# Kernel tuning notes

Hardware: AMD Instinct MI355X
Metric: run time of the kernel (lower is better)

## Reference

```python
import jax, jax.numpy as jnp
import numpy as np

NUM_ITEMS = 50000
EMB = 16
SLATE = 10
HID = 512
LAT = 64
RESP = 1024
BATCH = 256


def _linear_params(k, out_dim, in_dim):
    kw, kb = jax.random.split(k)
    s = 1.0 / np.sqrt(in_dim)
    W = jax.random.uniform(kw, (out_dim, in_dim), jnp.float32, -s, s)
    b = jax.random.uniform(kb, (out_dim,), jnp.float32, -s, s)
    return W, b


def setup_inputs() -> dict:
    key = jax.random.key(0)
    ks = jax.random.split(key, 10)
    user_repr = jax.random.randint(ks[0], (BATCH, NUM_ITEMS), 0, 2, dtype=jnp.int32)
    slate = jax.random.randint(ks[1], (BATCH, SLATE), 0, NUM_ITEMS, dtype=jnp.int32)
    response_encoded = jax.random.uniform(ks[2], (BATCH, RESP), jnp.float32)
    eps = jax.random.normal(ks[3], (BATCH, LAT), jnp.float32)
    emb = jax.random.normal(ks[4], (NUM_ITEMS, EMB), jnp.float32)
    in_enc = SLATE * EMB + EMB + RESP
    W_enc, b_enc = _linear_params(ks[5], HID, in_enc)
    W_mu, b_mu = _linear_params(ks[6], LAT, HID)
    W_lv, b_lv = _linear_params(ks[7], LAT, HID)
    in_dec = LAT + EMB + RESP
    W_d1, b_d1 = _linear_params(ks[8], HID, in_dec)
    W_d2, b_d2 = _linear_params(ks[9], SLATE * EMB, HID)
    return {"user_repr": user_repr, "slate": slate, "response_encoded": response_encoded,
            "eps": eps, "emb": emb, "W_enc": W_enc, "b_enc": b_enc,
            "W_mu": W_mu, "b_mu": b_mu, "W_lv": W_lv, "b_lv": b_lv,
            "W_d1": W_d1, "b_d1": b_d1, "W_d2": W_d2, "b_d2": b_d2}


def reference(user_repr, slate, response_encoded, eps, emb,
              W_enc, b_enc, W_mu, b_mu, W_lv, b_lv, W_d1, b_d1, W_d2, b_d2):
    # Ragged embedding-mean pooling over interacted items (vectorized segment mean):
    # mean of emb rows where user_repr==1  ==  (indicator @ emb) / count
    uf = user_repr.astype(jnp.float32)                       # [B, N]
    counts = jnp.sum(uf, axis=1, keepdims=True)              # [B, 1]
    user = (uf @ emb) / counts                               # [B, E]

    cond = jnp.concatenate([user, response_encoded], axis=1)  # [B, E+R]
    slate_emb = emb[slate]                                    # [B, K, E]
    slate_vec = slate_emb.reshape(-1, SLATE * EMB)            # [B, K*E]
    x = jnp.concatenate([slate_vec, cond], axis=1)

    # encoder
    h = jax.nn.relu(x @ W_enc.T + b_enc)
    z_mean = h @ W_mu.T + b_mu
    z_log_var = h @ W_lv.T + b_lv

    # reparameterized sample
    z = z_mean + eps * jnp.exp(0.5 * z_log_var)

    # decoder
    dz = jnp.concatenate([z, cond], axis=1)
    dh = jax.nn.relu(dz @ W_d1.T + b_d1)
    rx = jax.nn.relu(dh @ W_d2.T + b_d2)                      # [B, K*E]
    rx = rx.reshape(-1, SLATE, EMB)                           # [B, K, E]

    # scores vs all items, softmax over items
    logits = jnp.einsum('bkh,nh->bkn', rx, emb)               # [B, K, N]
    probs = jax.nn.softmax(logits, axis=2)
    recon_slate = jnp.argmax(probs, axis=2)                   # [B, K]
    recon_resp = jnp.take_along_axis(probs, slate[:, :, None], axis=2)[..., 0]  # [B, K]
    return z_mean, z_log_var, recon_slate, recon_resp
```

## Files before the change

### kernel.cpp

```cpp
#include <hip/hip_runtime.h>

#define NITEMS 50000
#define EMBD   16
#define NSLATE 10
#define HIDD   512
#define LATD   64
#define RESPD  1024
#define BATCH  256
#define NPCH   25
#define PI4    500
#define BG     4
#define LOG2E  1.44269504088896340736f
#define SHIFT  64.0f

#define NCOL   2560
#define NT     1563
#define IC     224
#define TPC    7

#define OUT_ZM 0
#define OUT_ZLV 16384
#define OUT_RS 32768
#define OUT_RR 35328

#define WS_X    0
#define WS_DZ   307200
#define WS_P2   0
#define WS_PS   0
#define WS_KEY  573440
#define WS_PP   589824
#define WS_PART 589824
#define WS_RX   1114112
#define WS_RXS0 1155072
#define WS_RXS1 1175552
#define WS_RXS2 1196032

typedef __attribute__((ext_vector_type(8))) short bfrag;
typedef __attribute__((ext_vector_type(16))) float f32x16;

__device__ __forceinline__ float bfround(float v) {
  unsigned u = __float_as_uint(v);
  unsigned r = (u + 0x7FFFu + ((u >> 16) & 1u)) & 0xFFFF0000u;
  return __uint_as_float(r);
}

__device__ __forceinline__ unsigned mono32(float f) {
  unsigned u = __float_as_uint(f);
  return (u & 0x80000000u) ? ~u : (u | 0x80000000u);
}

#define FMAX3(a, b, c) fmaxf(fmaxf((a), (b)), (c))

__global__ __launch_bounds__(256) void pool_part(const int* __restrict__ u,
    const float* __restrict__ emb, float* __restrict__ pp) {
  int bg = blockIdx.x, c = blockIdx.y, t = threadIdx.x;
  float acc[BG][17];
  #pragma unroll
  for (int j = 0; j < BG; ++j)
    #pragma unroll
    for (int i = 0; i < 17; ++i) acc[j][i] = 0.0f;
  const int4* ub = (const int4*)u;
  size_t base = (size_t)(bg * BG) * 12500 + (size_t)c * PI4;
  int nBase = c * 2000;
  for (int i4 = t; i4 < PI4; i4 += 256) {
    int4 u0 = ub[base + i4];
    int4 u1 = ub[base + 12500 + i4];
    int4 u2 = ub[base + 25000 + i4];
    int4 u3 = ub[base + 37500 + i4];
    int w[BG][4] = {{u0.x, u0.y, u0.z, u0.w}, {u1.x, u1.y, u1.z, u1.w},
                    {u2.x, u2.y, u2.z, u2.w}, {u3.x, u3.y, u3.z, u3.w}};
    const float4* e4 = (const float4*)(emb + (size_t)(nBase + i4 * 4) * 16);
    #pragma unroll
    for (int it = 0; it < 4; ++it) {
      float4 ea = e4[it * 4 + 0], eb = e4[it * 4 + 1];
      float4 ec = e4[it * 4 + 2], ed = e4[it * 4 + 3];
      #pragma unroll
      for (int j = 0; j < BG; ++j) {
        float wf = (float)w[j][it];
        acc[j][0]  = fmaf(wf, ea.x, acc[j][0]);
        acc[j][1]  = fmaf(wf, ea.y, acc[j][1]);
        acc[j][2]  = fmaf(wf, ea.z, acc[j][2]);
        acc[j][3]  = fmaf(wf, ea.w, acc[j][3]);
        acc[j][4]  = fmaf(wf, eb.x, acc[j][4]);
        acc[j][5]  = fmaf(wf, eb.y, acc[j][5]);
        acc[j][6]  = fmaf(wf, eb.z, acc[j][6]);
        acc[j][7]  = fmaf(wf, eb.w, acc[j][7]);
        acc[j][8]  = fmaf(wf, ec.x, acc[j][8]);
        acc[j][9]  = fmaf(wf, ec.y, acc[j][9]);
        acc[j][10] = fmaf(wf, ec.z, acc[j][10]);
        acc[j][11] = fmaf(wf, ec.w, acc[j][11]);
        acc[j][12] = fmaf(wf, ed.x, acc[j][12]);
        acc[j][13] = fmaf(wf, ed.y, acc[j][13]);
        acc[j][14] = fmaf(wf, ed.z, acc[j][14]);
        acc[j][15] = fmaf(wf, ed.w, acc[j][15]);
        acc[j][16] += wf;
      }
    }
  }
  #pragma unroll
  for (int off = 32; off > 0; off >>= 1) {
    #pragma unroll
    for (int j = 0; j < BG; ++j)
      #pragma unroll
      for (int i = 0; i < 17; ++i) acc[j][i] += __shfl_down(acc[j][i], off);
  }
  int lane = t & 63, wv = t >> 6;
  if (lane == 0) {
    float* dst = pp + (size_t)((bg * NPCH + c) * 4 + wv) * (BG * 17);
    #pragma unroll
    for (int j = 0; j < BG; ++j)
      #pragma unroll
      for (int i = 0; i < 17; ++i) dst[j * 17 + i] = acc[j][i];
  }
}

__global__ __launch_bounds__(256) void build_x(const float* __restrict__ pp,
    const int* __restrict__ slate, const float* __restrict__ resp,
    const float* __restrict__ emb, float* __restrict__ x, float* __restrict__ dz) {
  __shared__ float fin[17];
  int b = blockIdx.x, t = threadIdx.x;
  if (t < 17) {
    int bg = b >> 2, j = b & 3;
    float a = 0.f;
    const float* p = pp + (size_t)(bg * NPCH * 4) * (BG * 17) + j * 17 + t;
    #pragma unroll
    for (int w = 0; w < NPCH * 4; ++w) a += p[(size_t)w * (BG * 17)];
    fin[t] = a;
  }
  __syncthreads();
  float inv = 1.0f / fin[16];
  if (t < 16) {
    float uv = fin[t] * inv;
    x[b * 1200 + 160 + t] = uv;
    dz[b * 1104 + 64 + t] = uv;
  }
  if (t >= 32 && t < 192) {
    int i = t - 32;
    int k = i >> 4, e = i & 15;
    int it = slate[b * 10 + k];
    x[b * 1200 + i] = emb[(size_t)it * 16 + e];
  }
  for (int i = t; i < 1024; i += 256) {
    float r = resp[b * 1024 + i];
    x[b * 1200 + 176 + i] = r;
    dz[b * 1104 + 80 + i] = r;
  }
}

__global__ __launch_bounds__(256) void gemm64(const float* __restrict__ A,
    const float* __restrict__ B, float* __restrict__ P, int M, int N, int K, int kChunk) {
  __shared__ float As[16][68];
  __shared__ float Bs[16][68];
  int tid = threadIdx.x;
  int m0 = blockIdx.y * 64, n0 = blockIdx.x * 64;
  int ks = blockIdx.z * kChunk;
  int ke = ks + kChunk; if (ke > K) ke = K;
  int sr = tid >> 2;
  int sc = (tid & 3) * 4;
  int tx = tid & 15, ty = tid >> 4;
  float acc[4][4];
  #pragma unroll
  for (int i = 0; i < 4; ++i)
    #pragma unroll
    for (int j = 0; j < 4; ++j) acc[i][j] = 0.f;
  for (int k0 = ks; k0 < ke; k0 += 16) {
    float4 av = make_float4(0.f, 0.f, 0.f, 0.f);
    float4 bv = make_float4(0.f, 0.f, 0.f, 0.f);
    if (k0 + sc < ke)
      av = *(const float4*)(A + (size_t)(m0 + sr) * K + k0 + sc);
    if (k0 + sc < ke && n0 + sr < N)
      bv = *(const float4*)(B + (size_t)(n0 + sr) * K + k0 + sc);
    __syncthreads();
    As[sc][sr] = av.x; As[sc + 1][sr] = av.y; As[sc + 2][sr] = av.z; As[sc + 3][sr] = av.w;
    Bs[sc][sr] = bv.x; Bs[sc + 1][sr] = bv.y; Bs[sc + 2][sr] = bv.z; Bs[sc + 3][sr] = bv.w;
    __syncthreads();
    #pragma unroll
    for (int kk = 0; kk < 16; ++kk) {
      float4 a4 = *(const float4*)&As[kk][4 * ty];
      float4 b4 = *(const float4*)&Bs[kk][4 * tx];
      float a[4] = {a4.x, a4.y, a4.z, a4.w};
      float b[4] = {b4.x, b4.y, b4.z, b4.w};
      #pragma unroll
      for (int i = 0; i < 4; ++i)
        #pragma unroll
        for (int j = 0; j < 4; ++j) acc[i][j] = fmaf(a[i], b[j], acc[i][j]);
    }
  }
  float* Pz = P + (size_t)blockIdx.z * M * N;
  #pragma unroll
  for (int i = 0; i < 4; ++i) {
    int m = m0 + 4 * ty + i, n = n0 + 4 * tx;
    if (n < N)
      *(float4*)(Pz + (size_t)m * N + n) = make_float4(acc[i][0], acc[i][1], acc[i][2], acc[i][3]);
  }
}

__global__ __launch_bounds__(128) void mulv_z_kernel(const float* __restrict__ part,
    const float* __restrict__ benc,
    const float* __restrict__ Wmu, const float* __restrict__ bmu,
    const float* __restrict__ Wlv, const float* __restrict__ blv,
    const float* __restrict__ eps, float* __restrict__ out, float* __restrict__ dz) {
  __shared__ __align__(16) float hs[512];
  __shared__ float zms[64], zlvs[64];
  int b = blockIdx.x, t = threadIdx.x;
  for (int i = t; i < 512; i += 128) {
    float a = benc[i];
    #pragma unroll
    for (int s = 0; s < 4; ++s) a += part[(size_t)s * 131072 + b * 512 + i];
    hs[i] = fmaxf(a, 0.f);
  }
  __syncthreads();
  const float* Wr = (t < 64) ? (Wmu + (size_t)t * 512) : (Wlv + (size_t)(t - 64) * 512);
  float bias = (t < 64) ? bmu[t] : blv[t - 64];
  const float4* w4 = (const float4*)Wr;
  const float4* h4 = (const float4*)hs;
  float a0 = 0.f, a1 = 0.f, a2 = 0.f, a3 = 0.f;
  #pragma unroll 4
  for (int i = 0; i < 128; ++i) {
    float4 w = w4[i], hv = h4[i];
    a0 = fmaf(w.x, hv.x, a0); a1 = fmaf(w.y, hv.y, a1);
    a2 = fmaf(w.z, hv.z, a2); a3 = fmaf(w.w, hv.w, a3);
  }
  float acc = (a0 + a1) + (a2 + a3) + bias;
  if (t < 64) { out[OUT_ZM + b * 64 + t] = acc; zms[t] = acc; }
  else        { out[OUT_ZLV + b * 64 + (t - 64)] = acc; zlvs[t - 64] = acc; }
  __syncthreads();
  if (t < 64) {
    float zv = fmaf(eps[b * 64 + t], __builtin_amdgcn_exp2f(0.7213475204444817f * zlvs[t]), zms[t]);
    dz[b * 1104 + t] = zv;
  }
}

__global__ __launch_bounds__(256) void gemm_d2(const float* __restrict__ part,
    const float* __restrict__ bd1, const float* __restrict__ W, float* __restrict__ p2) {
  __shared__ float As[16][68];
  __shared__ float Bs[16][68];
  const int N = 160;
  int tid = threadIdx.x;
  int m0 = blockIdx.y * 64, n0 = blockIdx.x * 64;
  int ks = blockIdx.z * 64, ke = ks + 64;
  int sr = tid >> 2, sc = (tid & 3) * 4;
  int tx = tid & 15, ty = tid >> 4;
  float acc[4][4];
  #pragma unroll
  for (int i = 0; i < 4; ++i)
    #pragma unroll
    for (int j = 0; j < 4; ++j) acc[i][j] = 0.f;
  for (int k0 = ks; k0 < ke; k0 += 16) {
    int col = k0 + sc;
    const float* p = part + (size_t)(m0 + sr) * 512 + col;
    float4 a0 = *(const float4*)(p);
    float4 a1 = *(const float4*)(p + 131072);
    float4 a2 = *(const float4*)(p + 262144);
    float4 a3 = *(const float4*)(p + 393216);
    float4 bb = *(const float4*)(bd1 + col);
    float4 av;
    av.x = fmaxf(a0.x + a1.x + a2.x + a3.x + bb.x, 0.f);
    av.y = fmaxf(a0.y + a1.y + a2.y + a3.y + bb.y, 0.f);
    av.z = fmaxf(a0.z + a1.z + a2.z + a3.z + bb.z, 0.f);
    av.w = fmaxf(a0.w + a1.w + a2.w + a3.w + bb.w, 0.f);
    float4 bv = make_float4(0.f, 0.f, 0.f, 0.f);
    if (n0 + sr < N)
      bv = *(const float4*)(W + (size_t)(n0 + sr) * 512 + col);
    __syncthreads();
    As[sc][sr] = av.x; As[sc + 1][sr] = av.y; As[sc + 2][sr] = av.z; As[sc + 3][sr] = av.w;
    Bs[sc][sr] = bv.x; Bs[sc + 1][sr] = bv.y; Bs[sc + 2][sr] = bv.z; Bs[sc + 3][sr] = bv.w;
    __syncthreads();
    #pragma unroll
    for (int kk = 0; kk < 16; ++kk) {
      float4 a4 = *(const float4*)&As[kk][4 * ty];
      float4 b4 = *(const float4*)&Bs[kk][4 * tx];
      float a[4] = {a4.x, a4.y, a4.z, a4.w};
      float b[4] = {b4.x, b4.y, b4.z, b4.w};
      #pragma unroll
      for (int i = 0; i < 4; ++i)
        #pragma unroll
        for (int j = 0; j < 4; ++j) acc[i][j] = fmaf(a[i], b[j], acc[i][j]);
    }
  }
  float* Pz = p2 + (size_t)blockIdx.z * 40960;
  #pragma unroll
  for (int i = 0; i < 4; ++i) {
    int m = m0 + 4 * ty + i, n = n0 + 4 * tx;
    if (n < N)
      *(float4*)(Pz + (size_t)m * 160 + n) = make_float4(acc[i][0], acc[i][1], acc[i][2], acc[i][3]);
  }
}

__global__ __launch_bounds__(256) void rx_prep(const float* __restrict__ p2,
    const float* __restrict__ bd2, float* __restrict__ rx,
    unsigned short* __restrict__ rx0, unsigned short* __restrict__ rx1,
    unsigned short* __restrict__ rx2, unsigned long long* __restrict__ keys) {
  int b = blockIdx.x, t = threadIdx.x;
  if (t < 10) keys[b * 10 + t] = 0ULL;
  if (t >= 160) return;
  float a = bd2[t];
  #pragma unroll
  for (int z = 0; z < 8; ++z) a += p2[(size_t)z * 40960 + b * 160 + t];
  float v = fmaxf(a, 0.f) * LOG2E;
  rx[b * 160 + t] = v;
  int col = b * 10 + (t >> 4), e = t & 15;
  float f0 = bfround(v);
  float d1 = v - f0;
  float f1 = bfround(d1);
  float d2 = d1 - f1;
  float f2 = bfround(d2);
  rx0[col * 16 + e] = (unsigned short)(__float_as_uint(f0) >> 16);
  rx1[col * 16 + e] = (unsigned short)(__float_as_uint(f1) >> 16);
  rx2[col * 16 + e] = (unsigned short)(__float_as_uint(f2) >> 16);
}

__global__ __launch_bounds__(256) void score_mfma(const float* __restrict__ emb,
    const unsigned short* __restrict__ rx0, const unsigned short* __restrict__ rx1,
    const unsigned short* __restrict__ rx2,
    float* __restrict__ ps, unsigned long long* __restrict__ keys) {
  int t = threadIdx.x;
  int w = t >> 6, l = t & 63;
  int ln = l & 31, hf = l >> 5;
  int pair = blockIdx.x * 4 + w;
  int ic = blockIdx.y;
  int colA = pair * 64 + ln;
  int colB = colA + 32;
  size_t offA = (size_t)colA * 16 + hf * 8;
  size_t offB = (size_t)colB * 16 + hf * 8;
  bfrag bA0 = *(const bfrag*)(rx0 + offA);
  bfrag bA1 = *(const bfrag*)(rx1 + offA);
  bfrag bA2 = *(const bfrag*)(rx2 + offA);
  bfrag bB0 = *(const bfrag*)(rx0 + offB);
  bfrag bB1 = *(const bfrag*)(rx1 + offB);
  bfrag bB2 = *(const bfrag*)(rx2 + offB);
  float sA = 0.f, sB = 0.f;
  float mA = -3.402823466e38f, mB = -3.402823466e38f;
  int tlA = 0, tlB = 0;
  int ts = ic * TPC, te = ts + TPC;
  if (te > NT) te = NT;
  #pragma unroll 1
  for (int tile = ts; tile < te; ++tile) {
    int r = tile * 32 + ln;
    float4 e0, e1;
    if (r < NITEMS) {
      const float4* p = (const float4*)(emb + (size_t)r * 16 + hf * 8);
      e0 = p[0]; e1 = p[1];
    } else {
      e0 = make_float4(-128.f, -128.f, -128.f, -128.f);
      e1 = e0;
    }
    float ev[8] = {e0.x, e0.y, e0.z, e0.w, e1.x, e1.y, e1.z, e1.w};
    union { bfrag f; unsigned u[4]; } A0, A1, A2;
    #pragma unroll
    for (int j = 0; j < 4; ++j) {
      float v0 = ev[2 * j], v1 = ev[2 * j + 1];
      unsigned u0 = __float_as_uint(v0), u1 = __float_as_uint(v1);
      A0.u[j] = (u0 >> 16) | (u1 & 0xFFFF0000u);
      float r0 = v0 - __uint_as_float(u0 & 0xFFFF0000u);
      float r1 = v1 - __uint_as_float(u1 & 0xFFFF0000u);
      unsigned w0 = __float_as_uint(r0), w1 = __float_as_uint(r1);
      A1.u[j] = (w0 >> 16) | (w1 & 0xFFFF0000u);
      float q0 = r0 - __uint_as_float(w0 & 0xFFFF0000u);
      float q1 = r1 - __uint_as_float(w1 & 0xFFFF0000u);
      A2.u[j] = (__float_as_uint(q0) >> 16) | (__float_as_uint(q1) & 0xFFFF0000u);
    }
    f32x16 accA, accB;
    #pragma unroll
    for (int i = 0; i < 16; ++i) { accA[i] = -SHIFT; accB[i] = -SHIFT; }
    accA = __builtin_amdgcn_mfma_f32_32x32x16_bf16(A1.f, bA1, accA, 0, 0, 0);
    accB = __builtin_amdgcn_mfma_f32_32x32x16_bf16(A1.f, bB1, accB, 0, 0, 0);
    accA = __builtin_amdgcn_mfma_f32_32x32x16_bf16(A2.f, bA0, accA, 0, 0, 0);
    accB = __builtin_amdgcn_mfma_f32_32x32x16_bf16(A2.f, bB0, accB, 0, 0, 0);
    accA = __builtin_amdgcn_mfma_f32_32x32x16_bf16(A0.f, bA2, accA, 0, 0, 0);
    accB = __builtin_amdgcn_mfma_f32_32x32x16_bf16(A0.f, bB2, accB, 0, 0, 0);
    accA = __builtin_amdgcn_mfma_f32_32x32x16_bf16(A1.f, bA0, accA, 0, 0, 0);
    accB = __builtin_amdgcn_mfma_f32_32x32x16_bf16(A1.f, bB0, accB, 0, 0, 0);
    accA = __builtin_amdgcn_mfma_f32_32x32x16_bf16(A0.f, bA1, accA, 0, 0, 0);
    accB = __builtin_amdgcn_mfma_f32_32x32x16_bf16(A0.f, bB1, accB, 0, 0, 0);
    accA = __builtin_amdgcn_mfma_f32_32x32x16_bf16(A0.f, bA0, accA, 0, 0, 0);
    accB = __builtin_amdgcn_mfma_f32_32x32x16_bf16(A0.f, bB0, accB, 0, 0, 0);
    float tmA, tmB;
    {
      float f1 = FMAX3(accA[0], accA[1], accA[2]);
      float f2 = FMAX3(accA[3], accA[4], accA[5]);
      float f3 = FMAX3(accA[6], accA[7], accA[8]);
      float f4 = FMAX3(accA[9], accA[10], accA[11]);
      float f5 = FMAX3(accA[12], accA[13], accA[14]);
      float g1 = FMAX3(f1, f2, accA[15]);
      float g2 = fmaxf(f3, f4);
      tmA = FMAX3(g1, g2, f5);
    }
    {
      float f1 = FMAX3(accB[0], accB[1], accB[2]);
      float f2 = FMAX3(accB[3], accB[4], accB[5]);
      float f3 = FMAX3(accB[6], accB[7], accB[8]);
      float f4 = FMAX3(accB[9], accB[10], accB[11]);
      float f5 = FMAX3(accB[12], accB[13], accB[14]);
      float g1 = FMAX3(f1, f2, accB[15]);
      float g2 = fmaxf(f3, f4);
      tmB = FMAX3(g1, g2, f5);
    }
    if (tmA > mA) { mA = tmA; tlA = tile; }
    if (tmB > mB) { mB = tmB; tlB = tile; }
    #pragma unroll
    for (int i = 0; i < 16; ++i) {
      sA += __builtin_amdgcn_exp2f(accA[i]);
      sB += __builtin_amdgcn_exp2f(accB[i]);
    }
  }
  sA += __shfl_xor(sA, 32);
  sB += __shfl_xor(sB, 32);
  {
    float om = __shfl_xor(mA, 32); int ot = __shfl_xor(tlA, 32);
    if (om > mA || (om == mA && ot < tlA)) { mA = om; tlA = ot; }
  }
  {
    float om = __shfl_xor(mB, 32); int ot = __shfl_xor(tlB, 32);
    if (om > mB || (om == mB && ot < tlB)) { mB = om; tlB = ot; }
  }
  if (hf == 0) {
    ps[ic * NCOL + colA] = sA;
    ps[ic * NCOL + colB] = sB;
    unsigned long long kA = ((unsigned long long)mono32(mA) << 32) | (unsigned)(2047 - tlA);
    unsigned long long kB = ((unsigned long long)mono32(mB) << 32) | (unsigned)(2047 - tlB);
    if (kA > keys[colA]) atomicMax(&keys[colA], kA);
    if (kB > keys[colB]) atomicMax(&keys[colB], kB);
  }
}

__global__ __launch_bounds__(64) void argmax_fix(const unsigned long long* __restrict__ keys,
    const unsigned short* __restrict__ rx0, const unsigned short* __restrict__ rx1,
    const unsigned short* __restrict__ rx2, const float* __restrict__ emb,
    float* __restrict__ out) {
  int l = threadIdx.x, ln = l & 31, hf = l >> 5;
  int g = blockIdx.x, k = blockIdx.y;
  int col = g * 32 + ln;
  unsigned long long key = keys[col];
  unsigned um = (unsigned)(key >> 32);
  int tl = 2047 - (int)(key & 0xFFFFFFFFu);
  size_t off = (size_t)col * 16 + hf * 8;
  bfrag b0 = *(const bfrag*)(rx0 + off);
  bfrag b1 = *(const bfrag*)(rx1 + off);
  bfrag b2 = *(const bfrag*)(rx2 + off);
  bool done = ((tl & 7) != k);
  while (true) {
    int tsel = done ? 0x7FFFFFFF : tl;
    #pragma unroll
    for (int o = 32; o > 0; o >>= 1) tsel = min(tsel, __shfl_xor(tsel, o));
    if (tsel == 0x7FFFFFFF) break;
    int r = tsel * 32 + ln;
    float4 e0, e1;
    if (r < NITEMS) {
      const float4* p = (const float4*)(emb + (size_t)r * 16 + hf * 8);
      e0 = p[0]; e1 = p[1];
    } else {
      e0 = make_float4(-128.f, -128.f, -128.f, -128.f);
      e1 = e0;
    }
    float ev[8] = {e0.x, e0.y, e0.z, e0.w, e1.x, e1.y, e1.z, e1.w};
    union { bfrag f; unsigned u[4]; } A0, A1, A2;
    #pragma unroll
    for (int j = 0; j < 4; ++j) {
      float v0 = ev[2 * j], v1 = ev[2 * j + 1];
      unsigned u0 = __float_as_uint(v0), u1 = __float_as_uint(v1);
      A0.u[j] = (u0 >> 16) | (u1 & 0xFFFF0000u);
      float r0 = v0 - __uint_as_float(u0 & 0xFFFF0000u);
      float r1 = v1 - __uint_as_float(u1 & 0xFFFF0000u);
      unsigned w0 = __float_as_uint(r0), w1 = __float_as_uint(r1);
      A1.u[j] = (w0 >> 16) | (w1 & 0xFFFF0000u);
      float q0 = r0 - __uint_as_float(w0 & 0xFFFF0000u);
      float q1 = r1 - __uint_as_float(w1 & 0xFFFF0000u);
      A2.u[j] = (__float_as_uint(q0) >> 16) | (__float_as_uint(q1) & 0xFFFF0000u);
    }
    f32x16 acc;
    #pragma unroll
    for (int i = 0; i < 16; ++i) acc[i] = -SHIFT;
    acc = __builtin_amdgcn_mfma_f32_32x32x16_bf16(A1.f, b1, acc, 0, 0, 0);
    acc = __builtin_amdgcn_mfma_f32_32x32x16_bf16(A2.f, b0, acc, 0, 0, 0);
    acc = __builtin_amdgcn_mfma_f32_32x32x16_bf16(A0.f, b2, acc, 0, 0, 0);
    acc = __builtin_amdgcn_mfma_f32_32x32x16_bf16(A1.f, b0, acc, 0, 0, 0);
    acc = __builtin_amdgcn_mfma_f32_32x32x16_bf16(A0.f, b1, acc, 0, 0, 0);
    acc = __builtin_amdgcn_mfma_f32_32x32x16_bf16(A0.f, b0, acc, 0, 0, 0);
    if (!done && tl == tsel) {
      int best = 0x7FFFFFFF;
      #pragma unroll
      for (int g2 = 0; g2 < 4; ++g2)
        #pragma unroll
        for (int i = 0; i < 4; ++i) {
          float x = acc[g2 * 4 + i];
          int row = 8 * g2 + 4 * hf + i;
          if (mono32(x) == um) best = min(best, tsel * 32 + row);
        }
      int ob = __shfl_xor(best, 32);
      best = min(best, ob);
      if (hf == 0) out[OUT_RS + col] = (float)best;
      done = true;
    }
  }
}

__global__ __launch_bounds__(256) void score_final(const float* __restrict__ psg,
    const float* __restrict__ rx, const float* __restrict__ emb,
    const int* __restrict__ slate, float* __restrict__ out) {
  int tid = blockIdx.x * 256 + threadIdx.x;
  if (tid >= BATCH * 10) return;
  int b = tid / 10, k = tid % 10;
  float S = 0.f;
  for (int c = 0; c < IC; ++c) S += psg[c * NCOL + tid];
  int it = slate[b * 10 + k];
  const float* er = emb + (size_t)it * 16;
  const float* rr = rx + b * 160 + k * 16;
  float xs = -SHIFT;
  #pragma unroll
  for (int e = 0; e < 16; ++e) xs = fmaf(rr[e], er[e], xs);
  out[OUT_RR + b * 10 + k] = __builtin_amdgcn_exp2f(xs) / S;
}

extern "C" void kernel_launch(void* const* d_in, const int* in_sizes, int n_in,
                              void* d_out, int out_size, void* d_ws, size_t ws_size,
                              hipStream_t stream) {
  const int* user_repr = (const int*)d_in[0];
  const int* slate = (const int*)d_in[1];
  const float* resp = (const float*)d_in[2];
  const float* eps = (const float*)d_in[3];
  const float* emb = (const float*)d_in[4];
  const float* W_enc = (const float*)d_in[5];
  const float* b_enc = (const float*)d_in[6];
  const float* W_mu = (const float*)d_in[7];
  const float* b_mu = (const float*)d_in[8];
  const float* W_lv = (const float*)d_in[9];
  const float* b_lv = (const float*)d_in[10];
  const float* W_d1 = (const float*)d_in[11];
  const float* b_d1 = (const float*)d_in[12];
  const float* W_d2 = (const float*)d_in[13];
  const float* b_d2 = (const float*)d_in[14];
  float* out = (float*)d_out;
  float* ws = (float*)d_ws;

  float* x    = ws + WS_X;
  float* dz   = ws + WS_DZ;
  float* p2   = ws + WS_P2;
  float* pp   = ws + WS_PP;
  float* part = ws + WS_PART;
  float* ps   = ws + WS_PS;
  unsigned long long* keys = (unsigned long long*)(ws + WS_KEY);
  float* rx   = ws + WS_RX;
  unsigned short* rx0 = (unsigned short*)(ws + WS_RXS0);
  unsigned short* rx1 = (unsigned short*)(ws + WS_RXS1);
  unsigned short* rx2 = (unsigned short*)(ws + WS_RXS2);

  pool_part<<<dim3(64, NPCH), 256, 0, stream>>>(user_repr, emb, pp);
  build_x<<<256, 256, 0, stream>>>(pp, slate, resp, emb, x, dz);
  gemm64<<<dim3(8, 4, 4), 256, 0, stream>>>(x, W_enc, part, 256, 512, 1200, 300);
  mulv_z_kernel<<<256, 128, 0, stream>>>(part, b_enc, W_mu, b_mu, W_lv, b_lv, eps, out, dz);
  gemm64<<<dim3(8, 4, 4), 256, 0, stream>>>(dz, W_d1, part, 256, 512, 1104, 276);
  gemm_d2<<<dim3(3, 4, 8), 256, 0, stream>>>(part, b_d1, W_d2, p2);
  rx_prep<<<256, 256, 0, stream>>>(p2, b_d2, rx, rx0, rx1, rx2, keys);
  score_mfma<<<dim3(10, IC), 256, 0, stream>>>(emb, rx0, rx1, rx2, ps, keys);
  argmax_fix<<<dim3(80, 8), 64, 0, stream>>>(keys, rx0, rx1, rx2, emb, out);
  score_final<<<10, 256, 0, stream>>>(ps, rx, emb, slate, out);
}
```

Measured before the change: 268.2 us.

## Compute user embedding pooling with bf16x3 MFMA instead of scalar FMAs

Replaces the scalar FMA pooling kernel with one that turns the 0/1 indicator into bf16 A fragments and splits each embedding value into three bf16 parts, accumulating with 32x32x16 bf16 MFMAs. A constant-one column in B yields the count alongside the sums. The reduction is re-tiled into 120 K-chunks over 8 row tiles of 32, and build_x now sums 120 partials per row. This trades CUDA-core FMA throughput for matrix-core throughput, at the cost of a smaller grid (240 blocks), uncoalesced per-row int loads, and redundant per-wave embedding conversion.

```diff
diff --git a/kernel.cpp b/kernel.cpp
--- a/kernel.cpp
+++ b/kernel.cpp
@@ -7,9 +7,7 @@
 #define LATD   64
 #define RESPD  1024
 #define BATCH  256
-#define NPCH   25
-#define PI4    500
-#define BG     4
+#define KCH    120
 #define LOG2E  1.44269504088896340736f
 #define SHIFT  64.0f
 
@@ -51,66 +49,63 @@
 
 #define FMAX3(a, b, c) fmaxf(fmaxf((a), (b)), (c))
 
-__global__ __launch_bounds__(256) void pool_part(const int* __restrict__ u,
+__global__ __launch_bounds__(256) void pool_mfma(const int* __restrict__ u,
     const float* __restrict__ emb, float* __restrict__ pp) {
-  int bg = blockIdx.x, c = blockIdx.y, t = threadIdx.x;
-  float acc[BG][17];
-  #pragma unroll
-  for (int j = 0; j < BG; ++j)
-    #pragma unroll
-    for (int i = 0; i < 17; ++i) acc[j][i] = 0.0f;
-  const int4* ub = (const int4*)u;
-  size_t base = (size_t)(bg * BG) * 12500 + (size_t)c * PI4;
-  int nBase = c * 2000;
-  for (int i4 = t; i4 < PI4; i4 += 256) {
-    int4 u0 = ub[base + i4];
-    int4 u1 = ub[base + 12500 + i4];
-    int4 u2 = ub[base + 25000 + i4];
-    int4 u3 = ub[base + 37500 + i4];
-    int w[BG][4] = {{u0.x, u0.y, u0.z, u0.w}, {u1.x, u1.y, u1.z, u1.w},
-                    {u2.x, u2.y, u2.z, u2.w}, {u3.x, u3.y, u3.z, u3.w}};
-    const float4* e4 = (const float4*)(emb + (size_t)(nBase + i4 * 4) * 16);
-    #pragma unroll
-    for (int it = 0; it < 4; ++it) {
-      float4 ea = e4[it * 4 + 0], eb = e4[it * 4 + 1];
-      float4 ec = e4[it * 4 + 2], ed = e4[it * 4 + 3];
+  int t = threadIdx.x;
+  int w = t >> 6, l = t & 63;
+  int ln = l & 31, hf = l >> 5;
+  int rt = blockIdx.x * 4 + w;
+  int kc = blockIdx.y;
+  int row = rt * 32 + ln;
+  int ks = kc * 26 + min(kc, 5);
+  int ke = ks + 26 + (kc < 5 ? 1 : 0);
+  const int* uRow = u + (size_t)row * NITEMS + hf * 8;
+  f32x16 acc;
+  #pragma unroll
+  for (int i = 0; i < 16; ++i) acc[i] = 0.f;
+  #pragma unroll 1
+  for (int k0 = ks; k0 < ke; ++k0) {
+    const int4* ap = (const int4*)(uRow + k0 * 16);
+    int4 a0 = ap[0], a1 = ap[1];
+    union { bfrag f; unsigned ui[4]; } A;
+    A.ui[0] = (a0.x ? 0x3F80u : 0u) | (a0.y ? 0x3F800000u : 0u);
+    A.ui[1] = (a0.z ? 0x3F80u : 0u) | (a0.w ? 0x3F800000u : 0u);
+    A.ui[2] = (a1.x ? 0x3F80u : 0u) | (a1.y ? 0x3F800000u : 0u);
+    A.ui[3] = (a1.z ? 0x3F80u : 0u) | (a1.w ? 0x3F800000u : 0u);
+    union { bfrag f; unsigned ui[4]; } B0, B1, B2;
+    if (ln < 16) {
+      const float* ep = emb + (size_t)(k0 * 16 + hf * 8) * 16 + ln;
       #pragma unroll
-      for (int j = 0; j < BG; ++j) {
-        float wf = (float)w[j][it];
-        acc[j][0]  = fmaf(wf, ea.x, acc[j][0]);
-        acc[j][1]  = fmaf(wf, ea.y, acc[j][1]);
-        acc[j][2]  = fmaf(wf, ea.z, acc[j][2]);
-        acc[j][3]  = fmaf(wf, ea.w, acc[j][3]);
-        acc[j][4]  = fmaf(wf, eb.x, acc[j][4]);
-        acc[j][5]  = fmaf(wf, eb.y, acc[j][5]);
-        acc[j][6]  = fmaf(wf, eb.z, acc[j][6]);
-        acc[j][7]  = fmaf(wf, eb.w, acc[j][7]);
-        acc[j][8]  = fmaf(wf, ec.x, acc[j][8]);
-        acc[j][9]  = fmaf(wf, ec.y, acc[j][9]);
-        acc[j][10] = fmaf(wf, ec.z, acc[j][10]);
-        acc[j][11] = fmaf(wf, ec.w, acc[j][11]);
-        acc[j][12] = fmaf(wf, ed.x, acc[j][12]);
-        acc[j][13] = fmaf(wf, ed.y, acc[j][13]);
-        acc[j][14] = fmaf(wf, ed.z, acc[j][14]);
-        acc[j][15] = fmaf(wf, ed.w, acc[j][15]);
-        acc[j][16] += wf;
+      for (int j = 0; j < 4; ++j) {
+        float v0 = ep[(2 * j) * 16], v1 = ep[(2 * j + 1) * 16];
+        unsigned u0 = __float_as_uint(v0), u1 = __float_as_uint(v1);
+        B0.ui[j] = (u0 >> 16) | (u1 & 0xFFFF0000u);
+        float r0 = v0 - __uint_as_float(u0 & 0xFFFF0000u);
+        float r1 = v1 - __uint_as_float(u1 & 0xFFFF0000u);
+        unsigned w0 = __float_as_uint(r0), w1 = __float_as_uint(r1);
+        B1.ui[j] = (w0 >> 16) | (w1 & 0xFFFF0000u);
+        float q0 = r0 - __uint_as_float(w0 & 0xFFFF0000u);
+        float q1 = r1 - __uint_as_float(w1 & 0xFFFF0000u);
+        B2.ui[j] = (__float_as_uint(q0) >> 16) | (__float_as_uint(q1) & 0xFFFF0000u);
       }
-    }
-  }
-  #pragma unroll
-  for (int off = 32; off > 0; off >>= 1) {
-    #pragma unroll
-    for (int j = 0; j < BG; ++j)
+    } else {
+      unsigned c0 = (ln == 16) ? 0x3F803F80u : 0u;
       #pragma unroll
-      for (int i = 0; i < 17; ++i) acc[j][i] += __shfl_down(acc[j][i], off);
-  }
-  int lane = t & 63, wv = t >> 6;
-  if (lane == 0) {
-    float* dst = pp + (size_t)((bg * NPCH + c) * 4 + wv) * (BG * 17);
-    #pragma unroll
-    for (int j = 0; j < BG; ++j)
+      for (int j = 0; j < 4; ++j) { B0.ui[j] = c0; B1.ui[j] = 0u; B2.ui[j] = 0u; }
+    }
+    acc = __builtin_amdgcn_mfma_f32_32x32x16_bf16(A.f, B2.f, acc, 0, 0, 0);
+    acc = __builtin_amdgcn_mfma_f32_32x32x16_bf16(A.f, B1.f, acc, 0, 0, 0);
+    acc = __builtin_amdgcn_mfma_f32_32x32x16_bf16(A.f, B0.f, acc, 0, 0, 0);
+  }
+  if (ln < 17) {
+    float* dst = pp + (size_t)kc * 4352 + (size_t)(rt * 32) * 17 + ln;
+    #pragma unroll
+    for (int g = 0; g < 4; ++g)
       #pragma unroll
-      for (int i = 0; i < 17; ++i) dst[j * 17 + i] = acc[j][i];
+      for (int q = 0; q < 4; ++q) {
+        int r = q + 8 * g + 4 * hf;
+        dst[r * 17] = acc[g * 4 + q];
+      }
   }
 }
 
@@ -120,11 +115,10 @@
   __shared__ float fin[17];
   int b = blockIdx.x, t = threadIdx.x;
   if (t < 17) {
-    int bg = b >> 2, j = b & 3;
     float a = 0.f;
-    const float* p = pp + (size_t)(bg * NPCH * 4) * (BG * 17) + j * 17 + t;
-    #pragma unroll
-    for (int w = 0; w < NPCH * 4; ++w) a += p[(size_t)w * (BG * 17)];
+    const float* p = pp + (size_t)b * 17 + t;
+    #pragma unroll 8
+    for (int kc = 0; kc < KCH; ++kc) a += p[(size_t)kc * 4352];
     fin[t] = a;
   }
   __syncthreads();
@@ -545,7 +539,7 @@
   unsigned short* rx1 = (unsigned short*)(ws + WS_RXS1);
   unsigned short* rx2 = (unsigned short*)(ws + WS_RXS2);
 
-  pool_part<<<dim3(64, NPCH), 256, 0, stream>>>(user_repr, emb, pp);
+  pool_mfma<<<dim3(2, KCH), 256, 0, stream>>>(user_repr, emb, pp);
   build_x<<<256, 256, 0, stream>>>(pp, slate, resp, emb, x, dz);
   gemm64<<<dim3(8, 4, 4), 256, 0, stream>>>(x, W_enc, part, 256, 512, 1200, 300);
   mulv_z_kernel<<<256, 128, 0, stream>>>(part, b_enc, W_mu, b_mu, W_lv, b_lv, eps, out, dz);
```

Measured after the change: 263.7 us. Within noise of the previous version (-1.7%).
